# Kernel tuning notes

Hardware: AMD Instinct MI355X
Metric: run time of the kernel (lower is better)

## Reference

```python
import jax, jax.numpy as jnp
import numpy as np

B, C, O = 8, 32, 64
G_IN, G_OUT, G_F = 33, 15, 7
X, Y, K = 64, 64, 5
INIT_ADJUST = 0.1


def setup_inputs() -> dict:
    key = jax.random.key(0)
    k1, k2, k3, k4 = jax.random.split(key, 4)
    x = jax.random.normal(k1, (B, C, G_IN, X, Y), dtype=jnp.float32)
    # idx[i, f] = in_index_dict[g_i * h_f]; per output element the G_F group
    # translates are distinct, so sample without replacement per row.
    rows = [jax.random.permutation(k, G_IN)[:G_F] for k in jax.random.split(k2, G_OUT)]
    idx = jnp.stack(rows).astype(jnp.int32)  # [G_OUT, G_F]
    weight = jax.random.normal(k3, (O, C, G_F, K, K), dtype=jnp.float32) * INIT_ADJUST
    bias = jax.random.uniform(k4, (O,), dtype=jnp.float32)
    return {"x": x, "weight": weight, "bias": bias, "idx": idx}


def reference(x, weight, bias, idx):
    # Equivalent to: scatter weight into a depth-G_IN zero kernel per output
    # group element, concat over G_OUT, run full-depth VALID conv3d.
    # Direct form: out[b,o,i,x,y] = sum_{c,f,kh,kw} x[b,c,idx[i,f],x+kh,y+kw]*W[o,c,f,kh,kw]
    b, c, g_in, xx, yy = x.shape
    o, _, g_f, kh, kw = weight.shape
    g_out = idx.shape[0]
    xg = x[:, :, idx]                                   # [B, C, G_out, G_f, X, Y]
    xg = xg.transpose(0, 2, 1, 3, 4, 5).reshape(b * g_out, c * g_f, xx, yy)
    w = weight.reshape(o, c * g_f, kh, kw)
    out = jax.lax.conv_general_dilated(
        xg, w, window_strides=(1, 1), padding="VALID",
        dimension_numbers=("NCHW", "OIHW", "NCHW"))    # [B*G_out, O, X', Y']
    out = out.reshape(b, g_out, o, xx - kh + 1, yy - kw + 1).transpose(0, 2, 1, 3, 4)
    return out + bias[None, :, None, None, None]
```

## Files before the change

### kernel.cpp

```cpp
#include <hip/hip_runtime.h>
#include <hip/hip_bf16.h>

#define GF    7
#define TAPS  25
#define NCHNK 7
#define NTILE 10
#define TROWS 6
#define SROWS 10
#define NPOS  360
#define NF_   23
#define NGRP  35

typedef __attribute__((ext_vector_type(8)))  __bf16 bf16x8;
typedef __attribute__((ext_vector_type(8)))  unsigned short u16x8;
typedef __attribute__((ext_vector_type(4)))  float f32x4;

__device__ __forceinline__ f32x4 mfma16(u16x8 a, u16x8 b, f32x4 c) {
  return __builtin_amdgcn_mfma_f32_16x16x32_bf16(
      __builtin_bit_cast(bf16x8, a), __builtin_bit_cast(bf16x8, b), c, 0, 0, 0);
}

__device__ __forceinline__ void glds16(const unsigned short* g, unsigned short* l) {
  __builtin_amdgcn_global_load_lds(
      (__attribute__((address_space(1))) void*)g,
      (__attribute__((address_space(3))) void*)l, 16, 0, 0);
}

__global__ void wt_kernel(const float* __restrict__ w, unsigned short* __restrict__ wt) {
  int i = blockIdx.x * 256 + threadIdx.x;
  if (i >= TAPS * NCHNK * 64 * 32) return;
  int e   = i & 7;
  int s   = (i >> 3) & 3;
  int o   = (i >> 5) & 63;
  int ck  = (i >> 11) % NCHNK;
  int tap = i / (NCHNK * 64 * 32);
  int cc = ck * 32 + 8 * (s ^ ((o >> 1) & 3)) + e;
  int c = cc / GF, f = cc - GF * (cc / GF);
  float v = w[(size_t)o * (32 * GF * TAPS) + c * (GF * TAPS) + f * TAPS + tap];
  __bf16 hb = (__bf16)v;
  wt[i] = __builtin_bit_cast(unsigned short, hb);
}

__global__ void __launch_bounds__(256, 2)
conv_kernel(const float* __restrict__ x, const unsigned short* __restrict__ wt,
            const float* __restrict__ bias, const int* __restrict__ idx,
            float* __restrict__ out) {
  __shared__ __align__(16) unsigned short Xs[640 * 32];
  __shared__ __align__(16) unsigned short Ws[5 * 2048];

  const int bid0 = blockIdx.x;
  const int bid  = (bid0 & 7) * 150 + (bid0 >> 3);
  const int tile = bid % NTILE;
  const int g    = (bid / NTILE) % 15;
  const int b    = bid / (NTILE * 15);

  const int tid  = threadIdx.x;
  const int lane = tid & 63;
  const int wv   = tid >> 6;
  const int lo   = lane & 15;
  const int lk   = lane >> 4;
  const int col  = lane;

  auto issue_ws = [&](int gi) {
    const int ckp = gi / 5, khp = gi - 5 * (gi / 5);
#pragma unroll
    for (int t = 0; t < 5; ++t) {
      const int tap = khp * 5 + t;
      glds16(wt + (((size_t)(tap * NCHNK + ckp)) << 11) + tid * 8,
             &Ws[t * 2048 + wv * 512]);
    }
  };
  issue_ws(0);

  int p0[6];
  int pvalid = 0;
#pragma unroll
  for (int i = 0; i < 6; ++i) {
    int nf = wv + 4 * i;
    p0[i] = 0;
    if (nf < NF_) {
      int p  = nf * 16 + lo;
      int pc = (p < NPOS) ? p : 0;
      int ph = pc / 60;
      p0[i] = ph * 64 + (pc - 60 * ph);
      pvalid = i + 1;
    }
  }

  int aoff[4];
#pragma unroll
  for (int m = 0; m < 4; ++m)
    aoff[m] = (m * 16 + lo) * 32 + 8 * (lk ^ ((lo >> 1) & 3));

  f32x4 acc[4][6];
#pragma unroll
  for (int m = 0; m < 4; ++m)
#pragma unroll
    for (int i = 0; i < 6; ++i) acc[m][i] = f32x4{0.f, 0.f, 0.f, 0.f};

  const int r0 = tile * TROWS;

  for (int gi = 0; gi < NGRP; ++gi) {
    const int ck = gi / 5;
    const int kh = gi - 5 * ck;
    if (kh == 0) {
      int ib[8];
#pragma unroll
      for (int k = 0; k < 8; ++k) {
        int cc = ck * 32 + 8 * wv + k;
        int c = cc / GF, f = cc - GF * c;
        ib[k] = ((b * 32 + c) * 33 + idx[g * GF + f]) << 12;
      }
#pragma unroll
      for (int row = 0; row < SROWS; ++row) {
        int ga = (r0 + row) * 64 + col;
        u16x8 pk;
#pragma unroll
        for (int k = 0; k < 8; ++k) {
          float v = x[ib[k] + ga];
          pk[k] = __builtin_bit_cast(unsigned short, (__bf16)v);
        }
        int pos = row * 64 + col;
        *reinterpret_cast<u16x8*>(&Xs[pos * 32 + 8 * (wv ^ ((pos >> 1) & 3))]) = pk;
      }
    }
    __syncthreads();

#pragma unroll
    for (int kw = 0; kw < 5; ++kw) {
      u16x8 a[4], bf[6];
#pragma unroll
      for (int m = 0; m < 4; ++m)
        a[m] = *reinterpret_cast<const u16x8*>(&Ws[kw * 2048 + aoff[m]]);
      const int toff = kh * 64 + kw;
#pragma unroll
      for (int i = 0; i < 6; ++i)
        if (i < pvalid) {
          int pt = p0[i] + toff;
          bf[i] = *reinterpret_cast<const u16x8*>(
              &Xs[pt * 32 + 8 * (lk ^ ((pt >> 1) & 3))]);
        }
#pragma unroll
      for (int i = 0; i < 6; ++i)
        if (i < pvalid)
#pragma unroll
          for (int m = 0; m < 4; ++m)
            acc[m][i] = mfma16(a[m], bf[i], acc[m][i]);
    }
    __syncthreads();
    if (gi + 1 < NGRP) issue_ws(gi + 1);
  }

  float bv[4][4];
#pragma unroll
  for (int m = 0; m < 4; ++m)
#pragma unroll
    for (int v = 0; v < 4; ++v) bv[m][v] = bias[m * 16 + 4 * lk + v];

#pragma unroll
  for (int i = 0; i < 6; ++i) {
    if (i < pvalid) {
      int nf = wv + 4 * i;
      int p  = nf * 16 + lo;
      if (p < NPOS) {
        const size_t pb = (size_t)tile * NPOS + p;
#pragma unroll
        for (int m = 0; m < 4; ++m)
#pragma unroll
          for (int v = 0; v < 4; ++v) {
            int o = m * 16 + 4 * lk + v;
            out[((size_t)(b * 64 + o) * 15 + g) * 3600 + pb] = acc[m][i][v] + bv[m][v];
          }
      }
    }
  }
}

extern "C" void kernel_launch(void* const* d_in, const int* in_sizes, int n_in,
                              void* d_out, int out_size, void* d_ws, size_t ws_size,
                              hipStream_t stream) {
  const float* x      = (const float*)d_in[0];
  const float* weight = (const float*)d_in[1];
  const float* bias   = (const float*)d_in[2];
  const int*   idx    = (const int*)d_in[3];
  float* out = (float*)d_out;
  unsigned short* wt = (unsigned short*)d_ws;

  wt_kernel<<<(TAPS * NCHNK * 64 * 32 + 255) / 256, 256, 0, stream>>>(weight, wt);
  conv_kernel<<<8 * 15 * NTILE, 256, 0, stream>>>(x, wt, bias, idx, out);
}
```

Measured before the change: 307.2 us.

## Pre-pack input to bf16 channel-last layout and stream tiles via async LDS loads

```diff
diff --git a/kernel.cpp b/kernel.cpp
--- a/kernel.cpp
+++ b/kernel.cpp
@@ -34,19 +34,37 @@
   int o   = (i >> 5) & 63;
   int ck  = (i >> 11) % NCHNK;
   int tap = i / (NCHNK * 64 * 32);
-  int cc = ck * 32 + 8 * (s ^ ((o >> 1) & 3)) + e;
-  int c = cc / GF, f = cc - GF * (cc / GF);
-  float v = w[(size_t)o * (32 * GF * TAPS) + c * (GF * TAPS) + f * TAPS + tap];
+  int oct = s ^ ((o >> 1) & 3);
+  int c   = 8 * oct + e;
+  float v = w[((size_t)(o * 32 + c) * GF + ck) * TAPS + tap];
   __bf16 hb = (__bf16)v;
   wt[i] = __builtin_bit_cast(unsigned short, hb);
 }
 
+__global__ void xt_kernel(const float* __restrict__ x, unsigned short* __restrict__ xt) {
+  int blk = blockIdx.x;
+  int row = blk & 63;
+  int pl  = blk >> 6;
+  int tid = threadIdx.x;
+  int col = tid >> 2, oct = tid & 3;
+  int b = pl / 33, gin = pl - 33 * b;
+  const float* xp = x + (((size_t)b * 32 * 33 + gin) << 12) + row * 64 + col;
+  u16x8 pk;
+#pragma unroll
+  for (int e = 0; e < 8; ++e) {
+    float v = xp[(size_t)(8 * oct + e) * 135168];
+    pk[e] = __builtin_bit_cast(unsigned short, (__bf16)v);
+  }
+  int pos = row * 64 + col;
+  *reinterpret_cast<u16x8*>(
+      &xt[((size_t)pl << 17) + pos * 32 + 8 * (oct ^ ((pos >> 1) & 3))]) = pk;
+}
+
 __global__ void __launch_bounds__(256, 2)
-conv_kernel(const float* __restrict__ x, const unsigned short* __restrict__ wt,
+conv_kernel(const unsigned short* __restrict__ xt, const unsigned short* __restrict__ wt,
             const float* __restrict__ bias, const int* __restrict__ idx,
             float* __restrict__ out) {
-  __shared__ __align__(16) unsigned short Xs[640 * 32];
-  __shared__ __align__(16) unsigned short Ws[5 * 2048];
+  extern __shared__ __align__(16) unsigned short lds[];
 
   const int bid0 = blockIdx.x;
   const int bid  = (bid0 & 7) * 150 + (bid0 >> 3);
@@ -59,18 +77,32 @@
   const int wv   = tid >> 6;
   const int lo   = lane & 15;
   const int lk   = lane >> 4;
-  const int col  = lane;
+  const int r0   = tile * TROWS;
+
+  int g7[NCHNK];
+#pragma unroll
+  for (int f = 0; f < NCHNK; ++f) g7[f] = idx[g * GF + f];
+  asm volatile("s_waitcnt vmcnt(0) lgkmcnt(0)" ::: "memory");
 
   auto issue_ws = [&](int gi) {
     const int ckp = gi / 5, khp = gi - 5 * (gi / 5);
-#pragma unroll
-    for (int t = 0; t < 5; ++t) {
-      const int tap = khp * 5 + t;
-      glds16(wt + (((size_t)(tap * NCHNK + ckp)) << 11) + tid * 8,
-             &Ws[t * 2048 + wv * 512]);
-    }
+    unsigned short* dst = lds + 20480 + (gi & 1) * 10240;
+#pragma unroll
+    for (int t = 0; t < 5; ++t)
+      glds16(wt + (((khp * 5 + t) * NCHNK + ckp) << 11) + tid * 8,
+             dst + t * 2048 + wv * 512);
   };
+  auto issue_xs = [&](int ckp) {
+    const unsigned short* src =
+        xt + (((size_t)(b * 33 + g7[ckp])) << 17) + r0 * 2048 + wv * 5120 + lane * 8;
+#pragma unroll
+    for (int t = 0; t < 10; ++t)
+      glds16(src + t * 512, lds + wv * 5120 + t * 512);
+  };
+
   issue_ws(0);
+  issue_xs(0);
+  issue_ws(1);
 
   int p0[6];
   int pvalid = 0;
@@ -86,7 +118,6 @@
       pvalid = i + 1;
     }
   }
-
   int aoff[4];
 #pragma unroll
   for (int m = 0; m < 4; ++m)
@@ -98,57 +129,51 @@
 #pragma unroll
     for (int i = 0; i < 6; ++i) acc[m][i] = f32x4{0.f, 0.f, 0.f, 0.f};
 
-  const int r0 = tile * TROWS;
-
+  asm volatile("s_waitcnt vmcnt(5)" ::: "memory");
+  __builtin_amdgcn_s_barrier();
+
+#pragma unroll 1
   for (int gi = 0; gi < NGRP; ++gi) {
-    const int ck = gi / 5;
-    const int kh = gi - 5 * ck;
-    if (kh == 0) {
-      int ib[8];
-#pragma unroll
-      for (int k = 0; k < 8; ++k) {
-        int cc = ck * 32 + 8 * wv + k;
-        int c = cc / GF, f = cc - GF * c;
-        ib[k] = ((b * 32 + c) * 33 + idx[g * GF + f]) << 12;
-      }
-#pragma unroll
-      for (int row = 0; row < SROWS; ++row) {
-        int ga = (r0 + row) * 64 + col;
-        u16x8 pk;
-#pragma unroll
-        for (int k = 0; k < 8; ++k) {
-          float v = x[ib[k] + ga];
-          pk[k] = __builtin_bit_cast(unsigned short, (__bf16)v);
-        }
-        int pos = row * 64 + col;
-        *reinterpret_cast<u16x8*>(&Xs[pos * 32 + 8 * (wv ^ ((pos >> 1) & 3))]) = pk;
-      }
-    }
-    __syncthreads();
+    const int ck = gi / 5, kh = gi - 5 * (gi / 5);
+    const unsigned short* Wcur = lds + 20480 + (gi & 1) * 10240;
 
 #pragma unroll
     for (int kw = 0; kw < 5; ++kw) {
       u16x8 a[4], bf[6];
 #pragma unroll
       for (int m = 0; m < 4; ++m)
-        a[m] = *reinterpret_cast<const u16x8*>(&Ws[kw * 2048 + aoff[m]]);
+        a[m] = *reinterpret_cast<const u16x8*>(&Wcur[kw * 2048 + aoff[m]]);
       const int toff = kh * 64 + kw;
 #pragma unroll
       for (int i = 0; i < 6; ++i)
         if (i < pvalid) {
           int pt = p0[i] + toff;
           bf[i] = *reinterpret_cast<const u16x8*>(
-              &Xs[pt * 32 + 8 * (lk ^ ((pt >> 1) & 3))]);
+              &lds[pt * 32 + 8 * (lk ^ ((pt >> 1) & 3))]);
         }
+      __builtin_amdgcn_s_setprio(1);
 #pragma unroll
       for (int i = 0; i < 6; ++i)
         if (i < pvalid)
 #pragma unroll
           for (int m = 0; m < 4; ++m)
             acc[m][i] = mfma16(a[m], bf[i], acc[m][i]);
-    }
-    __syncthreads();
-    if (gi + 1 < NGRP) issue_ws(gi + 1);
+      __builtin_amdgcn_s_setprio(0);
+    }
+
+    if (gi == NGRP - 1) break;
+    if (kh == 4) {
+      asm volatile("s_waitcnt vmcnt(0)" ::: "memory");
+      __builtin_amdgcn_s_barrier();
+      issue_xs(ck + 1);
+      issue_ws(gi + 2);
+      asm volatile("s_waitcnt vmcnt(5)" ::: "memory");
+      __builtin_amdgcn_s_barrier();
+    } else {
+      asm volatile("s_waitcnt vmcnt(0)" ::: "memory");
+      __builtin_amdgcn_s_barrier();
+      if (gi + 2 < NGRP) issue_ws(gi + 2);
+    }
   }
 
   float bv[4][4];
@@ -185,7 +210,12 @@
   const int*   idx    = (const int*)d_in[3];
   float* out = (float*)d_out;
   unsigned short* wt = (unsigned short*)d_ws;
+  unsigned short* xt = (unsigned short*)d_ws + 358400;
+
+  (void)hipFuncSetAttribute(reinterpret_cast<const void*>(conv_kernel),
+                            hipFuncAttributeMaxDynamicSharedMemorySize, 81920);
 
   wt_kernel<<<(TAPS * NCHNK * 64 * 32 + 255) / 256, 256, 0, stream>>>(weight, wt);
-  conv_kernel<<<8 * 15 * NTILE, 256, 0, stream>>>(x, wt, bias, idx, out);
-}
+  xt_kernel<<<264 * 64, 256, 0, stream>>>(x, xt);
+  conv_kernel<<<8 * 15 * NTILE, 256, 81920, stream>>>(xt, wt, bias, idx, out);
+}
```

New measurement: 321.2 us. +4.6%, slower.
